# Optimization experiments

Measured on AMD Instinct MI355X. Metric: run time of the kernel, lower is better.

The kernel has to match this reference:

```python
import jax, jax.numpy as jnp
import numpy as np
import math

EPS = 1e-5
B, S, D = 4, 4096, 2048


def setup_inputs() -> dict:
    key = jax.random.key(0)
    x = jax.random.normal(key, (B, S, D, 2), dtype=jnp.float32)  # complex x as (real, imag)
    g = jnp.array([1.0 / math.sqrt(2.0), 0.0, 1.0 / math.sqrt(2.0)], dtype=jnp.float32)
    gamma = jnp.tile(g[None, :], (D, 1))            # (D,3), torch init
    beta = jnp.zeros((D, 2), dtype=jnp.float32)     # complex beta as (real, imag)
    return {"x": x, "gamma": gamma, "beta": beta}


def reference(x, gamma, beta):
    b, s, d, _ = x.shape
    bs = b * s
    # complex mean over hidden dim == per-channel mean of real/imag
    x = x - jnp.mean(x, axis=2, keepdims=True)
    xr = x.reshape(bs, d, 2)
    # per-token 2x2 covariance of (real, imag)
    var = jnp.einsum('kdi,kdj->kij', xr, xr) / (d - 1)          # (bs,2,2)
    var = var + EPS * jnp.eye(2, dtype=x.dtype)
    w, v = jnp.linalg.eigh(var)                                  # (bs,2), (bs,2,2)
    inv_sqrt_w = 1.0 / jnp.sqrt(w)
    # std_inv = V diag(1/sqrt(w)) V^{-1}
    std_inv = jnp.einsum('kij,kj,kjl->kil', v, inv_sqrt_w, jnp.linalg.inv(v))
    # whiten: (bs,2,2) @ (bs,2,d) -> (bs,2,d)
    xw = jnp.einsum('kij,kdj->kid', std_inv, xr)
    # d-major flatten exactly as torch permute(2,0,1).reshape(d*bs,2,1)
    xf = jnp.transpose(xw, (2, 0, 1)).reshape(d * bs, 2)
    # per-dim symmetric 2x2 affine: [[g0,g1],[g1,g2]]
    G = jnp.stack([gamma[:, :2], gamma[:, 1:]], axis=-1)         # (d,2,2)
    Gt = jnp.tile(G, (bs, 1, 1))                                 # (d*bs,2,2): element k -> G[k % d]
    y = jnp.einsum('kij,kj->ki', Gt, xf)                         # (d*bs,2)
    y = jnp.transpose(y.reshape(d, bs, 2), (1, 0, 2)) + beta[None, :, :]  # (bs,d,2)
    return y.reshape(b, s, d, 2)
```

## Files before the change

kernel.cpp:

```cpp
#include <hip/hip_runtime.h>


constexpr int D = 2048;
constexpr float EPSV = 1e-5f;

__global__ __launch_bounds__(256)
void spectral_ln_kernel(const float4* __restrict__ x4,
                        const float* __restrict__ gamma,
                        const float4* __restrict__ beta4,
                        float4* __restrict__ out4,
                        int n_tokens)
{
    const int lane = threadIdx.x & 63;
    const int wid  = threadIdx.x >> 6;
    const int tok  = blockIdx.x * 4 + wid;
    if (tok >= n_tokens) return;
    const long base = (long)tok * (D * 2 / 4);

    const float4* __restrict__ xin = x4 + base;
    float4 v[16];
#pragma unroll
    for (int j = 0; j < 16; ++j) v[j] = xin[j * 64 + lane];

    float sr = 0.f, si = 0.f, rr = 0.f, ri = 0.f, ii = 0.f;
#pragma unroll
    for (int j = 0; j < 16; ++j) {
        sr += v[j].x + v[j].z;  si += v[j].y + v[j].w;
        rr += v[j].x * v[j].x + v[j].z * v[j].z;
        ri += v[j].x * v[j].y + v[j].z * v[j].w;
        ii += v[j].y * v[j].y + v[j].w * v[j].w;
    }
#pragma unroll
    for (int o = 32; o > 0; o >>= 1) {
        sr += __shfl_xor(sr, o, 64);
        si += __shfl_xor(si, o, 64);
        rr += __shfl_xor(rr, o, 64);
        ri += __shfl_xor(ri, o, 64);
        ii += __shfl_xor(ii, o, 64);
    }

    const float invD = 1.0f / D, inv_dm1 = 1.0f / (D - 1);
    const float mu_r = sr * invD, mu_i = si * invD;
    const float a = (rr - sr * mu_r) * inv_dm1 + EPSV;
    const float b = (ri - sr * mu_i) * inv_dm1;
    const float c = (ii - si * mu_i) * inv_dm1 + EPSV;

    const float s   = sqrtf(a * c - b * b);
    const float t2  = sqrtf(a + c + 2.f * s);
    const float inv = 1.f / (s * t2);
    const float si00 = (c + s) * inv, si01 = -b * inv, si11 = (a + s) * inv;

    const int m = tok & (D - 1);
    const float g0 = gamma[m * 3 + 0], g1 = gamma[m * 3 + 1], g2 = gamma[m * 3 + 2];
    const float M00 = g0 * si00 + g1 * si01;
    const float M01 = g0 * si01 + g1 * si11;
    const float M10 = g1 * si00 + g2 * si01;
    const float M11 = g1 * si01 + g2 * si11;

    float4* __restrict__ op = out4 + base;
#pragma unroll
    for (int j = 0; j < 16; ++j) {
        const float4 bt = beta4[j * 64 + lane];
        const float cr0 = v[j].x - mu_r, ci0 = v[j].y - mu_i;
        const float cr1 = v[j].z - mu_r, ci1 = v[j].w - mu_i;
        float4 o4;
        o4.x = M00 * cr0 + M01 * ci0 + bt.x;
        o4.y = M10 * cr0 + M11 * ci0 + bt.y;
        o4.z = M00 * cr1 + M01 * ci1 + bt.z;
        o4.w = M10 * cr1 + M11 * ci1 + bt.w;
        op[j * 64 + lane] = o4;
    }
}

extern "C" void kernel_launch(void* const* d_in, const int* in_sizes, int n_in,
                              void* d_out, int out_size, void* d_ws, size_t ws_size,
                              hipStream_t stream) {
    const float4* x4    = (const float4*)d_in[0];
    const float*  gamma = (const float*)d_in[1];
    const float4* beta4 = (const float4*)d_in[2];
    float4* out4 = (float4*)d_out;
    const int n_tokens = in_sizes[0] / (D * 2);
    const int blocks = (n_tokens + 3) / 4;
    spectral_ln_kernel<<<dim3(blocks), dim3(256), 0, stream>>>(x4, gamma, beta4, out4, n_tokens);
}
```

Before: 436.3 us.

## Use one block per token with LDS cross-wave reduction and nontemporal I/O

Each token is now handled by a whole 256-thread block instead of one wavefront, so each thread holds 4 float4 values instead of 16 and the per-token statistics are combined across waves through shared memory and a barrier. Global input loads and output stores use nontemporal hints, beta is prefetched into registers up front, and launch bounds request higher occupancy. This is meant to cut register pressure and raise memory-level parallelism in a bandwidth-bound kernel, at the cost of a block-wide sync and more blocks to schedule.

```diff
diff --git a/kernel.cpp b/kernel.cpp
--- a/kernel.cpp
+++ b/kernel.cpp
@@ -1,30 +1,38 @@
 #include <hip/hip_runtime.h>
 
+
+typedef float f32x4 __attribute__((ext_vector_type(4)));
 
 constexpr int D = 2048;
 constexpr float EPSV = 1e-5f;
 
-__global__ __launch_bounds__(256)
-void spectral_ln_kernel(const float4* __restrict__ x4,
+__global__ __launch_bounds__(256, 8)
+void spectral_ln_kernel(const f32x4* __restrict__ x4,
                         const float* __restrict__ gamma,
-                        const float4* __restrict__ beta4,
-                        float4* __restrict__ out4,
-                        int n_tokens)
+                        const f32x4* __restrict__ beta4,
+                        f32x4* __restrict__ out4)
 {
-    const int lane = threadIdx.x & 63;
-    const int wid  = threadIdx.x >> 6;
-    const int tok  = blockIdx.x * 4 + wid;
-    if (tok >= n_tokens) return;
+    __shared__ float red[4][5];
+
+    const int tid  = threadIdx.x;
+    const int lane = tid & 63;
+    const int wid  = tid >> 6;
+    const int tok  = blockIdx.x;
     const long base = (long)tok * (D * 2 / 4);
 
-    const float4* __restrict__ xin = x4 + base;
-    float4 v[16];
+    const f32x4* __restrict__ xin = x4 + base;
+
+    f32x4 v[4], bt[4];
 #pragma unroll
-    for (int j = 0; j < 16; ++j) v[j] = xin[j * 64 + lane];
+    for (int j = 0; j < 4; ++j)
+        v[j] = __builtin_nontemporal_load(xin + j * 256 + tid);
+#pragma unroll
+    for (int j = 0; j < 4; ++j)
+        bt[j] = beta4[j * 256 + tid];
 
     float sr = 0.f, si = 0.f, rr = 0.f, ri = 0.f, ii = 0.f;
 #pragma unroll
-    for (int j = 0; j < 16; ++j) {
+    for (int j = 0; j < 4; ++j) {
         sr += v[j].x + v[j].z;  si += v[j].y + v[j].w;
         rr += v[j].x * v[j].x + v[j].z * v[j].z;
         ri += v[j].x * v[j].y + v[j].z * v[j].w;
@@ -38,6 +46,16 @@
         ri += __shfl_xor(ri, o, 64);
         ii += __shfl_xor(ii, o, 64);
     }
+    if (lane == 0) {
+        red[wid][0] = sr; red[wid][1] = si; red[wid][2] = rr;
+        red[wid][3] = ri; red[wid][4] = ii;
+    }
+    __syncthreads();
+    sr = red[0][0] + red[1][0] + red[2][0] + red[3][0];
+    si = red[0][1] + red[1][1] + red[2][1] + red[3][1];
+    rr = red[0][2] + red[1][2] + red[2][2] + red[3][2];
+    ri = red[0][3] + red[1][3] + red[2][3] + red[3][3];
+    ii = red[0][4] + red[1][4] + red[2][4] + red[3][4];
 
     const float invD = 1.0f / D, inv_dm1 = 1.0f / (D - 1);
     const float mu_r = sr * invD, mu_i = si * invD;
@@ -57,29 +75,27 @@
     const float M10 = g1 * si00 + g2 * si01;
     const float M11 = g1 * si01 + g2 * si11;
 
-    float4* __restrict__ op = out4 + base;
+    f32x4* __restrict__ op = out4 + base;
 #pragma unroll
-    for (int j = 0; j < 16; ++j) {
-        const float4 bt = beta4[j * 64 + lane];
+    for (int j = 0; j < 4; ++j) {
         const float cr0 = v[j].x - mu_r, ci0 = v[j].y - mu_i;
         const float cr1 = v[j].z - mu_r, ci1 = v[j].w - mu_i;
-        float4 o4;
-        o4.x = M00 * cr0 + M01 * ci0 + bt.x;
-        o4.y = M10 * cr0 + M11 * ci0 + bt.y;
-        o4.z = M00 * cr1 + M01 * ci1 + bt.z;
-        o4.w = M10 * cr1 + M11 * ci1 + bt.w;
-        op[j * 64 + lane] = o4;
+        f32x4 o4;
+        o4.x = M00 * cr0 + M01 * ci0 + bt[j].x;
+        o4.y = M10 * cr0 + M11 * ci0 + bt[j].y;
+        o4.z = M00 * cr1 + M01 * ci1 + bt[j].z;
+        o4.w = M10 * cr1 + M11 * ci1 + bt[j].w;
+        __builtin_nontemporal_store(o4, op + j * 256 + tid);
     }
 }
 
 extern "C" void kernel_launch(void* const* d_in, const int* in_sizes, int n_in,
                               void* d_out, int out_size, void* d_ws, size_t ws_size,
                               hipStream_t stream) {
-    const float4* x4    = (const float4*)d_in[0];
-    const float*  gamma = (const float*)d_in[1];
-    const float4* beta4 = (const float4*)d_in[2];
-    float4* out4 = (float4*)d_out;
+    const f32x4* x4    = (const f32x4*)d_in[0];
+    const float* gamma = (const float*)d_in[1];
+    const f32x4* beta4 = (const f32x4*)d_in[2];
+    f32x4* out4 = (f32x4*)d_out;
     const int n_tokens = in_sizes[0] / (D * 2);
-    const int blocks = (n_tokens + 3) / 4;
-    spectral_ln_kernel<<<dim3(blocks), dim3(256), 0, stream>>>(x4, gamma, beta4, out4, n_tokens);
+    spectral_ln_kernel<<<dim3(n_tokens), dim3(256), 0, stream>>>(x4, gamma, beta4, out4);
 }
```

New measurement: 417.8 us. 4.2% less time.
